# Kernel optimization log

Measured on AMD Instinct MI355X. Metric: run time of the kernel, lower is better.

## Reference

```python
import jax, jax.numpy as jnp
import numpy as np

N_NODES = 100000


def gcn_conv(x, W, b, src, dst, n_nodes):
    """PyG GCNConv: add self-loops, symmetric deg^-1/2 normalization,
    linear transform then gather->scale->scatter-add, plus bias."""
    h = x @ W  # [N, out] - transform first (small GEMM), propagate after
    loop = jnp.arange(n_nodes, dtype=src.dtype)
    s = jnp.concatenate([src, loop])  # sources incl. self-loops
    d = jnp.concatenate([dst, loop])  # targets incl. self-loops
    deg = jax.ops.segment_sum(jnp.ones_like(d, dtype=h.dtype), d,
                              num_segments=n_nodes)  # in-degree on augmented graph
    dinv = jnp.where(deg > 0, jax.lax.rsqrt(deg), 0.0)
    norm = dinv[s] * dinv[d]  # [E+N]
    msg = h[s] * norm[:, None]  # gather + per-edge scale
    out = jax.ops.segment_sum(msg, d, num_segments=n_nodes)  # scatter-add
    return out + b


def setup_inputs() -> dict:
    key = jax.random.key(0)
    ks = jax.random.split(key, 8)
    in_dim, hid = 128, 128
    n_edges = 1600000
    x = jax.random.normal(ks[0], (N_NODES, in_dim), dtype=jnp.float32)
    edge_index = jax.random.randint(ks[1], (2, n_edges), 0, N_NODES, dtype=jnp.int64)
    s1 = 1.0 / np.sqrt(in_dim)
    s2 = 1.0 / np.sqrt(hid)
    W1 = jax.random.uniform(ks[2], (in_dim, hid), jnp.float32, -s1, s1)
    b1 = jnp.zeros((hid,), jnp.float32)
    W2 = jax.random.uniform(ks[3], (hid, 2), jnp.float32, -s2, s2)
    b2 = jnp.zeros((2,), jnp.float32)
    W_skip = jax.random.uniform(ks[4], (in_dim, 2), jnp.float32, -s1, s1)
    b_skip = jnp.zeros((2,), jnp.float32)
    return {"x": x, "edge_index": edge_index, "W1": W1, "b1": b1,
            "W2": W2, "b2": b2, "W_skip": W_skip, "b_skip": b_skip}


def reference(x, edge_index, W1, b1, W2, b2, W_skip, b_skip):
    src, dst = edge_index[0], edge_index[1]
    h = gcn_conv(x, W1, b1, src, dst, N_NODES)
    h = jax.nn.relu(h)
    # dropout is identity in eval mode (training=False)
    out = gcn_conv(h, W2, b2, src, dst, N_NODES)
    out = out + x @ W_skip + b_skip
    return out
```

## Files before the change

kernel.cpp:

```cpp
#include <hip/hip_runtime.h>

#define NN 100000
#define NB 196
#define BSHIFT 9
#define BMASK 511

typedef __attribute__((ext_vector_type(8))) short short8;
typedef __attribute__((ext_vector_type(4))) float f32x4;

__device__ __forceinline__ unsigned short f2bf(float f) {
  union { float f; unsigned int u; } v;
  v.f = f;
  unsigned int r = (v.u + 0x7fffu + ((v.u >> 16) & 1u)) >> 16;
  return (unsigned short)r;
}
__device__ __forceinline__ float bf_lo(unsigned int u) {
  union { unsigned int u; float f; } v;
  v.u = u << 16;
  return v.f;
}
__device__ __forceinline__ float bf_hi(unsigned int u) {
  union { unsigned int u; float f; } v;
  v.u = u & 0xffff0000u;
  return v.f;
}

__global__ __launch_bounds__(256) void k_bucket(const float* __restrict__ W1,
                                                unsigned short* __restrict__ pw,
                                                const int* __restrict__ src,
                                                const int* __restrict__ dst, int E,
                                                int cap, int* __restrict__ bcur,
                                                unsigned int* __restrict__ bkt) {
  if (blockIdx.x < 8) {
    int idx = blockIdx.x * 256 + threadIdx.x;
    int lane = idx & 63, f = idx >> 6;
    int nt = f >> 2, ks = f & 3;
    int n = nt * 16 + (lane & 15);
    int k0 = ks * 32 + (lane >> 4) * 8;
    unsigned short tmp[8];
#pragma unroll
    for (int j = 0; j < 8; ++j) tmp[j] = f2bf(W1[(k0 + j) * 128 + n]);
    *(uint4*)&pw[idx * 8] = *(uint4*)tmp;
    return;
  }
  __shared__ int cnt_l[NB];
  __shared__ int start_l[NB];
  __shared__ int gbase[NB];
  __shared__ unsigned int stage[2048];
  __shared__ int addr[2048];
  const int t = threadIdx.x;
  for (int i = t; i < NB; i += 256) cnt_l[i] = 0;
  __syncthreads();
  const int nblk = gridDim.x - 8;
  const int nbatch = (E + 2047) >> 11;
  for (int bi = blockIdx.x - 8; bi < nbatch; bi += nblk) {
    const int e0 = bi << 11;
    unsigned int ent[8];
    int bb[8], pp[8];
#pragma unroll
    for (int j = 0; j < 8; ++j) {
      int e = e0 + j * 256 + t;
      if (e < E) {
        int d = dst[e], s = src[e];
        bb[j] = d >> BSHIFT;
        ent[j] = ((unsigned int)s << BSHIFT) | (unsigned int)(d & BMASK);
        pp[j] = atomicAdd(&cnt_l[bb[j]], 1);
      } else {
        bb[j] = -1;
      }
    }
    __syncthreads();
    if (t < NB) gbase[t] = atomicAdd(&bcur[t], cnt_l[t]);
    if (t == 0) {
      int run = 0;
      for (int b = 0; b < NB; ++b) { start_l[b] = run; run += cnt_l[b]; }
    }
    __syncthreads();
#pragma unroll
    for (int j = 0; j < 8; ++j) {
      if (bb[j] >= 0) {
        int slot = start_l[bb[j]] + pp[j];
        stage[slot] = ent[j];
        addr[slot] = bb[j] * cap + gbase[bb[j]] + pp[j];
      }
    }
    __syncthreads();
    int totaln = start_l[NB - 1] + cnt_l[NB - 1];
    for (int s = t; s < totaln; s += 256) bkt[addr[s]] = stage[s];
    __syncthreads();
    for (int i = t; i < NB; i += 256) cnt_l[i] = 0;
    __syncthreads();
  }
}

__global__ __launch_bounds__(256) void k_bcount(const int* __restrict__ bcur,
                                                const unsigned int* __restrict__ bkt,
                                                int cap, int* __restrict__ cnt, int n) {
  __shared__ int hist[512];
  const int b = blockIdx.x;
  for (int i = threadIdx.x; i < 512; i += 256) hist[i] = 0;
  __syncthreads();
  const int m = bcur[b];
  const unsigned int* p = &bkt[(size_t)b * cap];
  for (int i = threadIdx.x; i < m; i += 256) atomicAdd(&hist[p[i] & BMASK], 1);
  __syncthreads();
  for (int i = threadIdx.x; i < 512; i += 256) {
    int node = (b << BSHIFT) + i;
    if (node < n) cnt[node] = hist[i];
  }
}

__global__ __launch_bounds__(256) void k_alloc(const int* __restrict__ cnt,
                                               int* __restrict__ ofs,
                                               float* __restrict__ dinv,
                                               int* __restrict__ total, int n) {
  int i = blockIdx.x * 256 + threadIdx.x;
  int c = (i < n) ? cnt[i] : 0;
  int cp = (c + 7) & ~7;
  if (i < n) dinv[i] = rsqrtf((float)c + 1.0f);
  const int lane = threadIdx.x & 63;
  const int wid = threadIdx.x >> 6;
  int incl = cp;
#pragma unroll
  for (int off = 1; off < 64; off <<= 1) {
    int v = __shfl_up(incl, off);
    if (lane >= off) incl += v;
  }
  __shared__ int wsum[4];
  __shared__ int base;
  if (lane == 63) wsum[wid] = incl;
  __syncthreads();
  if (threadIdx.x == 0) {
    int s0 = wsum[0], s1 = wsum[1], s2 = wsum[2], s3 = wsum[3];
    base = atomicAdd(total, s0 + s1 + s2 + s3);
    wsum[0] = 0; wsum[1] = s0; wsum[2] = s0 + s1; wsum[3] = s0 + s1 + s2;
  }
  __syncthreads();
  if (i < n) ofs[i] = base + wsum[wid] + incl - cp;
}

__global__ __launch_bounds__(256) void k_scatter(const int* __restrict__ bcur,
                                                 const unsigned int* __restrict__ bkt,
                                                 int cap, const int* __restrict__ ofs,
                                                 int* __restrict__ bin, int n) {
  __shared__ int cur[512];
  __shared__ int ofs_l[512];
  const int b = blockIdx.x;
  for (int i = threadIdx.x; i < 512; i += 256) {
    cur[i] = 0;
    int node = (b << BSHIFT) + i;
    ofs_l[i] = (node < n) ? ofs[node] : 0;
  }
  __syncthreads();
  const int m = bcur[b];
  const unsigned int* p = &bkt[(size_t)b * cap];
  for (int i = threadIdx.x; i < m; i += 256) {
    unsigned int u = p[i];
    int dl = u & BMASK;
    int pos = atomicAdd(&cur[dl], 1);
    bin[ofs_l[dl] + pos] = (int)(u >> BSHIFT);
  }
  __syncthreads();
  for (int i = threadIdx.x; i < 512; i += 256) {
    int node = (b << BSHIFT) + i;
    if (node < n) {
      int c = cur[i];
      int cp = (c + 7) & ~7;
      int basei = ofs_l[i];
      for (int p2 = c; p2 < cp; ++p2) bin[basei + p2] = n;
    }
  }
}

__global__ __launch_bounds__(256) void k_gemm1(const float* __restrict__ x,
                                               const uint4* __restrict__ pw4,
                                               const float* __restrict__ W_skip,
                                               const float* __restrict__ dinv,
                                               unsigned short* __restrict__ hA16,
                                               float* __restrict__ skipout, int N) {
  __shared__ __align__(16) unsigned short Bs[16384];
  __shared__ float Ws[256];
  const int t = threadIdx.x;
#pragma unroll
  for (int it = 0; it < 8; ++it) {
    int idx = t + it * 256;
    *(uint4*)&Bs[idx * 8] = pw4[idx];
  }
  Ws[t] = W_skip[t];
  __syncthreads();

  const int lane = t & 63, w = t >> 6;
  const int m = lane & 15, q = lane >> 4;
  const int grow = blockIdx.x * 64 + w * 16 + m;
  const bool valid = grow < N;
  const float* xp = &x[(size_t)(valid ? grow : 0) * 128];

  f32x4 acc[8];
#pragma unroll
  for (int nt = 0; nt < 8; ++nt) acc[nt] = (f32x4){0.f, 0.f, 0.f, 0.f};
  float sk0 = 0.f, sk1 = 0.f;

#pragma unroll
  for (int ks = 0; ks < 4; ++ks) {
    short8 a;
    const int kb = ks * 32 + q * 8;
    if (valid) {
      const float* p = xp + kb;
      float4 f0 = *(const float4*)p;
      float4 f1 = *(const float4*)(p + 4);
      a[0] = (short)f2bf(f0.x); a[1] = (short)f2bf(f0.y);
      a[2] = (short)f2bf(f0.z); a[3] = (short)f2bf(f0.w);
      a[4] = (short)f2bf(f1.x); a[5] = (short)f2bf(f1.y);
      a[6] = (short)f2bf(f1.z); a[7] = (short)f2bf(f1.w);
      sk0 += f0.x * Ws[(kb + 0) * 2] + f0.y * Ws[(kb + 1) * 2] +
             f0.z * Ws[(kb + 2) * 2] + f0.w * Ws[(kb + 3) * 2] +
             f1.x * Ws[(kb + 4) * 2] + f1.y * Ws[(kb + 5) * 2] +
             f1.z * Ws[(kb + 6) * 2] + f1.w * Ws[(kb + 7) * 2];
      sk1 += f0.x * Ws[(kb + 0) * 2 + 1] + f0.y * Ws[(kb + 1) * 2 + 1] +
             f0.z * Ws[(kb + 2) * 2 + 1] + f0.w * Ws[(kb + 3) * 2 + 1] +
             f1.x * Ws[(kb + 4) * 2 + 1] + f1.y * Ws[(kb + 5) * 2 + 1] +
             f1.z * Ws[(kb + 6) * 2 + 1] + f1.w * Ws[(kb + 7) * 2 + 1];
    } else {
      a = (short8)0;
    }
#pragma unroll
    for (int nt = 0; nt < 8; ++nt) {
      short8 bfr = *(const short8*)&Bs[((nt * 4 + ks) * 64 + lane) * 8];
      acc[nt] = __builtin_amdgcn_mfma_f32_16x16x32_bf16(a, bfr, acc[nt], 0, 0, 0);
    }
  }

  sk0 += __shfl_xor(sk0, 16); sk0 += __shfl_xor(sk0, 32);
  sk1 += __shfl_xor(sk1, 16); sk1 += __shfl_xor(sk1, 32);
  if (valid && q == 0) *(float2*)&skipout[grow * 2] = make_float2(sk0, sk1);

  const int orow = blockIdx.x * 64 + w * 16 + q * 4;
  float4 dv = *(const float4*)&dinv[orow];
  float dvr[4] = {dv.x, dv.y, dv.z, dv.w};
#pragma unroll
  for (int nt = 0; nt < 8; ++nt) {
    int col = nt * 16 + m;
#pragma unroll
    for (int rg = 0; rg < 4; ++rg) {
      int rr = orow + rg;
      if (rr < N) hA16[(size_t)rr * 128 + col] = f2bf(acc[nt][rg] * dvr[rg]);
    }
  }
}

__global__ __launch_bounds__(256) void k_gather1(const int* __restrict__ ofs,
                                                 const int* __restrict__ cnt,
                                                 const int* __restrict__ bin,
                                                 const float* __restrict__ dinv,
                                                 const uint4* __restrict__ hp,
                                                 const float* __restrict__ b1,
                                                 const float* __restrict__ W2,
                                                 float* __restrict__ t2s, int N) {
  int d = blockIdx.x * 4 + (threadIdx.x >> 6);
  if (d >= N) return;
  const int lane = threadIdx.x & 63;
  const int rg = lane >> 4;
  const int fl = lane & 15;
  const int beg = ofs[d];
  const int np = (cnt[d] + 7) & ~7;

  const float dd = dinv[d];
  uint4 vs = hp[(size_t)d * 16 + fl];
  float4 b1a = *(const float4*)&b1[fl * 8];
  float4 b1b = *(const float4*)&b1[fl * 8 + 4];
  float4 wa = *(const float4*)&W2[fl * 16];
  float4 wb = *(const float4*)&W2[fl * 16 + 4];
  float4 wc = *(const float4*)&W2[fl * 16 + 8];
  float4 wd = *(const float4*)&W2[fl * 16 + 12];

  float acc[8] = {};
  for (int e0 = 0; e0 < np; e0 += 8) {
    int s0 = bin[beg + e0 + rg];
    int s1 = bin[beg + e0 + 4 + rg];
    uint4 v0 = hp[(size_t)s0 * 16 + fl];
    uint4 v1 = hp[(size_t)s1 * 16 + fl];
    acc[0] += bf_lo(v0.x); acc[1] += bf_hi(v0.x);
    acc[2] += bf_lo(v0.y); acc[3] += bf_hi(v0.y);
    acc[4] += bf_lo(v0.z); acc[5] += bf_hi(v0.z);
    acc[6] += bf_lo(v0.w); acc[7] += bf_hi(v0.w);
    acc[0] += bf_lo(v1.x); acc[1] += bf_hi(v1.x);
    acc[2] += bf_lo(v1.y); acc[3] += bf_hi(v1.y);
    acc[4] += bf_lo(v1.z); acc[5] += bf_hi(v1.z);
    acc[6] += bf_lo(v1.w); acc[7] += bf_hi(v1.w);
  }
#pragma unroll
  for (int j = 0; j < 8; ++j) {
    acc[j] += __shfl_xor(acc[j], 16);
    acc[j] += __shfl_xor(acc[j], 32);
  }
  acc[0] += bf_lo(vs.x); acc[1] += bf_hi(vs.x);
  acc[2] += bf_lo(vs.y); acc[3] += bf_hi(vs.y);
  acc[4] += bf_lo(vs.z); acc[5] += bf_hi(vs.z);
  acc[6] += bf_lo(vs.w); acc[7] += bf_hi(vs.w);

  float vj[8];
  vj[0] = fmaxf(acc[0] * dd + b1a.x, 0.f);
  vj[1] = fmaxf(acc[1] * dd + b1a.y, 0.f);
  vj[2] = fmaxf(acc[2] * dd + b1a.z, 0.f);
  vj[3] = fmaxf(acc[3] * dd + b1a.w, 0.f);
  vj[4] = fmaxf(acc[4] * dd + b1b.x, 0.f);
  vj[5] = fmaxf(acc[5] * dd + b1b.y, 0.f);
  vj[6] = fmaxf(acc[6] * dd + b1b.z, 0.f);
  vj[7] = fmaxf(acc[7] * dd + b1b.w, 0.f);
  float p0 = vj[0] * wa.x + vj[1] * wa.z + vj[2] * wb.x + vj[3] * wb.z +
             vj[4] * wc.x + vj[5] * wc.z + vj[6] * wd.x + vj[7] * wd.z;
  float p1 = vj[0] * wa.y + vj[1] * wa.w + vj[2] * wb.y + vj[3] * wb.w +
             vj[4] * wc.y + vj[5] * wc.w + vj[6] * wd.y + vj[7] * wd.w;
#pragma unroll
  for (int off = 1; off < 16; off <<= 1) {
    p0 += __shfl_xor(p0, off);
    p1 += __shfl_xor(p1, off);
  }
  if (lane == 0) *(float2*)&t2s[d * 2] = make_float2(p0 * dd, p1 * dd);
}

__global__ __launch_bounds__(256) void k_final(const float* __restrict__ b_skip,
                                               const float* __restrict__ b2,
                                               const float* __restrict__ t2s,
                                               const float* __restrict__ skipout,
                                               const float* __restrict__ dinv,
                                               const int* __restrict__ ofs,
                                               const int* __restrict__ cnt,
                                               const int* __restrict__ bin,
                                               float* __restrict__ out, int N) {
  int i = blockIdx.x * 4 + (threadIdx.x >> 6);
  if (i >= N) return;
  const int lane = threadIdx.x & 63;
  const int beg = ofs[i], end = beg + cnt[i];
  float g0 = 0.f, g1 = 0.f;
  for (int e = beg + lane; e < end; e += 64) {
    int s = bin[e];
    float2 t = *(const float2*)&t2s[s * 2];
    g0 += t.x; g1 += t.y;
  }
#pragma unroll
  for (int off = 32; off > 0; off >>= 1) {
    g0 += __shfl_down(g0, off);
    g1 += __shfl_down(g1, off);
  }
  if (lane == 0) {
    float di = dinv[i];
    float2 ts = *(const float2*)&t2s[i * 2];
    float2 sk = *(const float2*)&skipout[i * 2];
    float o0 = di * (g0 + ts.x) + b2[0] + sk.x + b_skip[0];
    float o1 = di * (g1 + ts.y) + b2[1] + sk.y + b_skip[1];
    *(float2*)&out[i * 2] = make_float2(o0, o1);
  }
}

extern "C" void kernel_launch(void* const* d_in, const int* in_sizes, int n_in,
                              void* d_out, int out_size, void* d_ws, size_t ws_size,
                              hipStream_t stream) {
  const float* x      = (const float*)d_in[0];
  const int*   edges  = (const int*)d_in[1];
  const float* W1     = (const float*)d_in[2];
  const float* b1     = (const float*)d_in[3];
  const float* W2     = (const float*)d_in[4];
  const float* b2     = (const float*)d_in[5];
  const float* W_skip = (const float*)d_in[6];
  const float* b_skip = (const float*)d_in[7];
  float* out = (float*)d_out;

  const int N = NN;
  const int E = in_sizes[1] / 2;
  const int* src = edges;
  const int* dst = edges + E;
  const size_t BINCAP = (size_t)E + 8 * (size_t)N;
  const int CAP = (((E + NB - 1) / NB) + 1280 + 255) & ~255;

  unsigned short* hA16 = (unsigned short*)d_ws;
  int*   bcur    = (int*)(hA16 + (size_t)(NN + 1) * 128);
  int*   total   = bcur + NB;
  int*   ofs     = total + 4;
  float* dinv    = (float*)(ofs + N + 4);
  int*   cnt     = (int*)(dinv + N);
  unsigned int* bkt = (unsigned int*)(cnt + N);
  int*   bin     = (int*)(bkt + (size_t)NB * CAP);
  float* t2s     = (float*)(bin + BINCAP);
  float* skipout = t2s + 2 * (size_t)N;
  unsigned short* pw = (unsigned short*)(skipout + 2 * (size_t)N);

  hipMemsetAsync(hA16 + (size_t)N * 128, 0, 256 + (NB + 4) * sizeof(int), stream);

  k_bucket<<<8 + 392, 256, 0, stream>>>(W1, pw, src, dst, E, CAP, bcur, bkt);
  k_bcount<<<NB, 256, 0, stream>>>(bcur, bkt, CAP, cnt, N);
  k_alloc<<<(N + 255) / 256, 256, 0, stream>>>(cnt, ofs, dinv, total, N);
  k_scatter<<<NB, 256, 0, stream>>>(bcur, bkt, CAP, ofs, bin, N);
  k_gemm1<<<(N + 63) / 64, 256, 0, stream>>>(x, (const uint4*)pw, W_skip, dinv, hA16,
                                             skipout, N);
  k_gather1<<<(N + 3) / 4, 256, 0, stream>>>(ofs, cnt, bin, dinv, (const uint4*)hA16,
                                             b1, W2, t2s, N);
  k_final<<<(N + 3) / 4, 256, 0, stream>>>(b_skip, b2, t2s, skipout, dinv, ofs, cnt,
                                           bin, out, N);
}
```

Baseline: 267.6 us.

## Fuse CSR count/alloc/scatter kernels, parallel-scan bucket offsets, packed-add gather

Merges the bucket-count, offset-allocation and scatter kernels into one per-bucket kernel that builds the histogram, scans padded counts, writes ofs/cnt/dinv and fills bins. This removes two launches and a global round-trip of the counts. The serial per-batch prefix loop in k_bucket becomes a wave shuffle scan, and the bucket grid is doubled. Padding grows to 16 so the layer-1 gather handles four neighbours per iteration with v_pk_add_f32 packed accumulation. The cost is more padding slots in the bin array and more gather loads on padded zero rows.

```diff
diff --git a/kernel.cpp b/kernel.cpp
--- a/kernel.cpp
+++ b/kernel.cpp
@@ -7,6 +7,7 @@
 
 typedef __attribute__((ext_vector_type(8))) short short8;
 typedef __attribute__((ext_vector_type(4))) float f32x4;
+typedef __attribute__((ext_vector_type(2))) float f32x2;
 
 __device__ __forceinline__ unsigned short f2bf(float f) {
   union { float f; unsigned int u; } v;
@@ -23,6 +24,18 @@
   union { unsigned int u; float f; } v;
   v.u = u & 0xffff0000u;
   return v.f;
+}
+__device__ __forceinline__ f32x2 mk2(unsigned int u) {
+  union { unsigned int u; float f; } lo, hi;
+  lo.u = u << 16;
+  hi.u = u & 0xffff0000u;
+  f32x2 r;
+  r.x = lo.f;
+  r.y = hi.f;
+  return r;
+}
+__device__ __forceinline__ void pkadd(f32x2& a, f32x2 b) {
+  asm("v_pk_add_f32 %0, %0, %1" : "+v"(a) : "v"(b));
 }
 
 __global__ __launch_bounds__(256) void k_bucket(const float* __restrict__ W1,
@@ -46,9 +59,11 @@
   __shared__ int cnt_l[NB];
   __shared__ int start_l[NB];
   __shared__ int gbase[NB];
+  __shared__ int wsum2[4];
   __shared__ unsigned int stage[2048];
   __shared__ int addr[2048];
   const int t = threadIdx.x;
+  const int lane = t & 63, wid = t >> 6;
   for (int i = t; i < NB; i += 256) cnt_l[i] = 0;
   __syncthreads();
   const int nblk = gridDim.x - 8;
@@ -70,11 +85,21 @@
       }
     }
     __syncthreads();
-    if (t < NB) gbase[t] = atomicAdd(&bcur[t], cnt_l[t]);
-    if (t == 0) {
-      int run = 0;
-      for (int b = 0; b < NB; ++b) { start_l[b] = run; run += cnt_l[b]; }
-    }
+    int v = (t < NB) ? cnt_l[t] : 0;
+    if (t < NB) gbase[t] = atomicAdd(&bcur[t], v);
+    int incl = v;
+#pragma unroll
+    for (int off = 1; off < 64; off <<= 1) {
+      int u = __shfl_up(incl, off);
+      if (lane >= off) incl += u;
+    }
+    if (lane == 63) wsum2[wid] = incl;
+    __syncthreads();
+    int wpre = 0;
+#pragma unroll
+    for (int j = 0; j < 4; ++j) wpre += (j < wid) ? wsum2[j] : 0;
+    int tot = wsum2[0] + wsum2[1] + wsum2[2] + wsum2[3];
+    if (t < NB) start_l[t] = wpre + incl - v;
     __syncthreads();
 #pragma unroll
     for (int j = 0; j < 8; ++j) {
@@ -85,90 +110,75 @@
       }
     }
     __syncthreads();
-    int totaln = start_l[NB - 1] + cnt_l[NB - 1];
-    for (int s = t; s < totaln; s += 256) bkt[addr[s]] = stage[s];
+    for (int s2 = t; s2 < tot; s2 += 256) bkt[addr[s2]] = stage[s2];
     __syncthreads();
     for (int i = t; i < NB; i += 256) cnt_l[i] = 0;
     __syncthreads();
   }
 }
 
-__global__ __launch_bounds__(256) void k_bcount(const int* __restrict__ bcur,
-                                                const unsigned int* __restrict__ bkt,
-                                                int cap, int* __restrict__ cnt, int n) {
+__global__ __launch_bounds__(256) void k_scatter(const int* __restrict__ bcur,
+                                                 const unsigned int* __restrict__ bkt,
+                                                 int cap, int* __restrict__ total,
+                                                 int* __restrict__ ofs,
+                                                 int* __restrict__ cnt,
+                                                 float* __restrict__ dinv,
+                                                 int* __restrict__ bin, int n) {
   __shared__ int hist[512];
+  __shared__ int sofs[512];
+  __shared__ int wsum[4];
+  __shared__ int base;
   const int b = blockIdx.x;
-  for (int i = threadIdx.x; i < 512; i += 256) hist[i] = 0;
+  const int t = threadIdx.x;
+  const int lane = t & 63, wid = t >> 6;
+  hist[2 * t] = 0;
+  hist[2 * t + 1] = 0;
   __syncthreads();
   const int m = bcur[b];
   const unsigned int* p = &bkt[(size_t)b * cap];
-  for (int i = threadIdx.x; i < m; i += 256) atomicAdd(&hist[p[i] & BMASK], 1);
-  __syncthreads();
-  for (int i = threadIdx.x; i < 512; i += 256) {
-    int node = (b << BSHIFT) + i;
-    if (node < n) cnt[node] = hist[i];
-  }
-}
-
-__global__ __launch_bounds__(256) void k_alloc(const int* __restrict__ cnt,
-                                               int* __restrict__ ofs,
-                                               float* __restrict__ dinv,
-                                               int* __restrict__ total, int n) {
-  int i = blockIdx.x * 256 + threadIdx.x;
-  int c = (i < n) ? cnt[i] : 0;
-  int cp = (c + 7) & ~7;
-  if (i < n) dinv[i] = rsqrtf((float)c + 1.0f);
-  const int lane = threadIdx.x & 63;
-  const int wid = threadIdx.x >> 6;
-  int incl = cp;
+  for (int i = t; i < m; i += 256) atomicAdd(&hist[p[i] & BMASK], 1);
+  __syncthreads();
+  int c0 = hist[2 * t], c1 = hist[2 * t + 1];
+  int cp0 = (c0 + 15) & ~15, cp1 = (c1 + 15) & ~15;
+  int v = cp0 + cp1;
+  int incl = v;
 #pragma unroll
   for (int off = 1; off < 64; off <<= 1) {
-    int v = __shfl_up(incl, off);
-    if (lane >= off) incl += v;
-  }
-  __shared__ int wsum[4];
-  __shared__ int base;
+    int u = __shfl_up(incl, off);
+    if (lane >= off) incl += u;
+  }
   if (lane == 63) wsum[wid] = incl;
   __syncthreads();
-  if (threadIdx.x == 0) {
+  if (t == 0) {
     int s0 = wsum[0], s1 = wsum[1], s2 = wsum[2], s3 = wsum[3];
     base = atomicAdd(total, s0 + s1 + s2 + s3);
     wsum[0] = 0; wsum[1] = s0; wsum[2] = s0 + s1; wsum[3] = s0 + s1 + s2;
   }
   __syncthreads();
-  if (i < n) ofs[i] = base + wsum[wid] + incl - cp;
-}
-
-__global__ __launch_bounds__(256) void k_scatter(const int* __restrict__ bcur,
-                                                 const unsigned int* __restrict__ bkt,
-                                                 int cap, const int* __restrict__ ofs,
-                                                 int* __restrict__ bin, int n) {
-  __shared__ int cur[512];
-  __shared__ int ofs_l[512];
-  const int b = blockIdx.x;
-  for (int i = threadIdx.x; i < 512; i += 256) {
-    cur[i] = 0;
-    int node = (b << BSHIFT) + i;
-    ofs_l[i] = (node < n) ? ofs[node] : 0;
-  }
-  __syncthreads();
-  const int m = bcur[b];
-  const unsigned int* p = &bkt[(size_t)b * cap];
-  for (int i = threadIdx.x; i < m; i += 256) {
+  int exc = base + wsum[wid] + incl - v;
+  sofs[2 * t] = exc;
+  sofs[2 * t + 1] = exc + cp0;
+  int node = (b << BSHIFT) + 2 * t;
+  if (node < n) {
+    ofs[node] = exc;
+    cnt[node] = c0;
+    dinv[node] = rsqrtf((float)c0 + 1.0f);
+  }
+  if (node + 1 < n) {
+    ofs[node + 1] = exc + cp0;
+    cnt[node + 1] = c1;
+    dinv[node + 1] = rsqrtf((float)c1 + 1.0f);
+  }
+  hist[2 * t] = 0;
+  hist[2 * t + 1] = 0;
+  __syncthreads();
+  for (int p2 = c0; p2 < cp0; ++p2) bin[exc + p2] = n;
+  for (int p2 = c1; p2 < cp1; ++p2) bin[exc + cp0 + p2] = n;
+  for (int i = t; i < m; i += 256) {
     unsigned int u = p[i];
     int dl = u & BMASK;
-    int pos = atomicAdd(&cur[dl], 1);
-    bin[ofs_l[dl] + pos] = (int)(u >> BSHIFT);
-  }
-  __syncthreads();
-  for (int i = threadIdx.x; i < 512; i += 256) {
-    int node = (b << BSHIFT) + i;
-    if (node < n) {
-      int c = cur[i];
-      int cp = (c + 7) & ~7;
-      int basei = ofs_l[i];
-      for (int p2 = c; p2 < cp; ++p2) bin[basei + p2] = n;
-    }
+    int pos = atomicAdd(&hist[dl], 1);
+    bin[sofs[dl] + pos] = (int)(u >> BSHIFT);
   }
 }
 
@@ -262,7 +272,7 @@
   const int rg = lane >> 4;
   const int fl = lane & 15;
   const int beg = ofs[d];
-  const int np = (cnt[d] + 7) & ~7;
+  const int np = (cnt[d] + 15) & ~15;
 
   const float dd = dinv[d];
   uint4 vs = hp[(size_t)d * 16 + fl];
@@ -273,21 +283,31 @@
   float4 wc = *(const float4*)&W2[fl * 16 + 8];
   float4 wd = *(const float4*)&W2[fl * 16 + 12];
 
-  float acc[8] = {};
-  for (int e0 = 0; e0 < np; e0 += 8) {
-    int s0 = bin[beg + e0 + rg];
-    int s1 = bin[beg + e0 + 4 + rg];
+  f32x2 a2[4];
+#pragma unroll
+  for (int j = 0; j < 4; ++j) a2[j] = (f32x2){0.f, 0.f};
+
+  for (int e0 = 0; e0 < np; e0 += 16) {
+    int eb = beg + e0 + rg;
+    int s0 = bin[eb], s1 = bin[eb + 4], s2 = bin[eb + 8], s3 = bin[eb + 12];
     uint4 v0 = hp[(size_t)s0 * 16 + fl];
     uint4 v1 = hp[(size_t)s1 * 16 + fl];
-    acc[0] += bf_lo(v0.x); acc[1] += bf_hi(v0.x);
-    acc[2] += bf_lo(v0.y); acc[3] += bf_hi(v0.y);
-    acc[4] += bf_lo(v0.z); acc[5] += bf_hi(v0.z);
-    acc[6] += bf_lo(v0.w); acc[7] += bf_hi(v0.w);
-    acc[0] += bf_lo(v1.x); acc[1] += bf_hi(v1.x);
-    acc[2] += bf_lo(v1.y); acc[3] += bf_hi(v1.y);
-    acc[4] += bf_lo(v1.z); acc[5] += bf_hi(v1.z);
-    acc[6] += bf_lo(v1.w); acc[7] += bf_hi(v1.w);
-  }
+    uint4 v2 = hp[(size_t)s2 * 16 + fl];
+    uint4 v3 = hp[(size_t)s3 * 16 + fl];
+    pkadd(a2[0], mk2(v0.x)); pkadd(a2[1], mk2(v0.y));
+    pkadd(a2[2], mk2(v0.z)); pkadd(a2[3], mk2(v0.w));
+    pkadd(a2[0], mk2(v1.x)); pkadd(a2[1], mk2(v1.y));
+    pkadd(a2[2], mk2(v1.z)); pkadd(a2[3], mk2(v1.w));
+    pkadd(a2[0], mk2(v2.x)); pkadd(a2[1], mk2(v2.y));
+    pkadd(a2[2], mk2(v2.z)); pkadd(a2[3], mk2(v2.w));
+    pkadd(a2[0], mk2(v3.x)); pkadd(a2[1], mk2(v3.y));
+    pkadd(a2[2], mk2(v3.z)); pkadd(a2[3], mk2(v3.w));
+  }
+  float acc[8];
+  acc[0] = a2[0].x; acc[1] = a2[0].y;
+  acc[2] = a2[1].x; acc[3] = a2[1].y;
+  acc[4] = a2[2].x; acc[5] = a2[2].y;
+  acc[6] = a2[3].x; acc[7] = a2[3].y;
 #pragma unroll
   for (int j = 0; j < 8; ++j) {
     acc[j] += __shfl_xor(acc[j], 16);
@@ -370,7 +390,7 @@
   const int E = in_sizes[1] / 2;
   const int* src = edges;
   const int* dst = edges + E;
-  const size_t BINCAP = (size_t)E + 8 * (size_t)N;
+  const size_t BINCAP = (size_t)E + 16 * (size_t)N;
   const int CAP = (((E + NB - 1) / NB) + 1280 + 255) & ~255;
 
   unsigned short* hA16 = (unsigned short*)d_ws;
@@ -387,10 +407,8 @@
 
   hipMemsetAsync(hA16 + (size_t)N * 128, 0, 256 + (NB + 4) * sizeof(int), stream);
 
-  k_bucket<<<8 + 392, 256, 0, stream>>>(W1, pw, src, dst, E, CAP, bcur, bkt);
-  k_bcount<<<NB, 256, 0, stream>>>(bcur, bkt, CAP, cnt, N);
-  k_alloc<<<(N + 255) / 256, 256, 0, stream>>>(cnt, ofs, dinv, total, N);
-  k_scatter<<<NB, 256, 0, stream>>>(bcur, bkt, CAP, ofs, bin, N);
+  k_bucket<<<8 + 784, 256, 0, stream>>>(W1, pw, src, dst, E, CAP, bcur, bkt);
+  k_scatter<<<NB, 256, 0, stream>>>(bcur, bkt, CAP, total, ofs, cnt, dinv, bin, N);
   k_gemm1<<<(N + 63) / 64, 256, 0, stream>>>(x, (const uint4*)pw, W_skip, dinv, hA16,
                                              skipout, N);
   k_gather1<<<(N + 3) / 4, 256, 0, stream>>>(ofs, cnt, bin, dinv, (const uint4*)hA16,
```

Result: no change. 265.0 us (-1.0%).

## Fuse bucket count, offset allocation and scatter; parallelize bucket prefix scan

Applied to the files above, without the earlier changes.

Merges the per-bucket histogram, offset allocation (with dinv) and scatter into one 512-thread kernel per bucket, reading each bucket's entries from its local histogram. The serial single-thread prefix over 196 buckets in the bucketing kernel becomes a wave-shuffle scan. Bucketing also moves to 512-thread blocks with 4096-edge batches and one block per batch. This removes two kernel launches and a global round trip for counts and offsets. In exchange, node offsets are allocated in bucket-block order rather than a global node order.

```diff
diff --git a/kernel.cpp b/kernel.cpp
--- a/kernel.cpp
+++ b/kernel.cpp
@@ -25,14 +25,14 @@
   return v.f;
 }
 
-__global__ __launch_bounds__(256) void k_bucket(const float* __restrict__ W1,
+__global__ __launch_bounds__(512) void k_bucket(const float* __restrict__ W1,
                                                 unsigned short* __restrict__ pw,
                                                 const int* __restrict__ src,
                                                 const int* __restrict__ dst, int E,
                                                 int cap, int* __restrict__ bcur,
                                                 unsigned int* __restrict__ bkt) {
-  if (blockIdx.x < 8) {
-    int idx = blockIdx.x * 256 + threadIdx.x;
+  if (blockIdx.x < 4) {
+    int idx = blockIdx.x * 512 + threadIdx.x;
     int lane = idx & 63, f = idx >> 6;
     int nt = f >> 2, ks = f & 3;
     int n = nt * 16 + (lane & 15);
@@ -46,20 +46,22 @@
   __shared__ int cnt_l[NB];
   __shared__ int start_l[NB];
   __shared__ int gbase[NB];
-  __shared__ unsigned int stage[2048];
-  __shared__ int addr[2048];
+  __shared__ int wsum2[8];
+  __shared__ unsigned int stage[4096];
+  __shared__ int addr[4096];
   const int t = threadIdx.x;
-  for (int i = t; i < NB; i += 256) cnt_l[i] = 0;
-  __syncthreads();
-  const int nblk = gridDim.x - 8;
-  const int nbatch = (E + 2047) >> 11;
-  for (int bi = blockIdx.x - 8; bi < nbatch; bi += nblk) {
-    const int e0 = bi << 11;
+  const int lane = t & 63, wid = t >> 6;
+  for (int i = t; i < NB; i += 512) cnt_l[i] = 0;
+  __syncthreads();
+  const int nblk = gridDim.x - 4;
+  const int nbatch = (E + 4095) >> 12;
+  for (int bi = blockIdx.x - 4; bi < nbatch; bi += nblk) {
+    const int e0 = bi << 12;
     unsigned int ent[8];
     int bb[8], pp[8];
 #pragma unroll
     for (int j = 0; j < 8; ++j) {
-      int e = e0 + j * 256 + t;
+      int e = e0 + j * 512 + t;
       if (e < E) {
         int d = dst[e], s = src[e];
         bb[j] = d >> BSHIFT;
@@ -70,11 +72,22 @@
       }
     }
     __syncthreads();
-    if (t < NB) gbase[t] = atomicAdd(&bcur[t], cnt_l[t]);
-    if (t == 0) {
-      int run = 0;
-      for (int b = 0; b < NB; ++b) { start_l[b] = run; run += cnt_l[b]; }
-    }
+    int v = (t < NB) ? cnt_l[t] : 0;
+    if (t < NB) gbase[t] = atomicAdd(&bcur[t], v);
+    int incl = v;
+#pragma unroll
+    for (int off = 1; off < 64; off <<= 1) {
+      int u = __shfl_up(incl, off);
+      if (lane >= off) incl += u;
+    }
+    if (lane == 63) wsum2[wid] = incl;
+    __syncthreads();
+    int wpre = 0;
+#pragma unroll
+    for (int j = 0; j < 8; ++j) wpre += (j < wid) ? wsum2[j] : 0;
+    int tot = wsum2[0] + wsum2[1] + wsum2[2] + wsum2[3] +
+              wsum2[4] + wsum2[5] + wsum2[6] + wsum2[7];
+    if (t < NB) start_l[t] = wpre + incl - v;
     __syncthreads();
 #pragma unroll
     for (int j = 0; j < 8; ++j) {
@@ -85,90 +98,66 @@
       }
     }
     __syncthreads();
-    int totaln = start_l[NB - 1] + cnt_l[NB - 1];
-    for (int s = t; s < totaln; s += 256) bkt[addr[s]] = stage[s];
-    __syncthreads();
-    for (int i = t; i < NB; i += 256) cnt_l[i] = 0;
-    __syncthreads();
-  }
-}
-
-__global__ __launch_bounds__(256) void k_bcount(const int* __restrict__ bcur,
-                                                const unsigned int* __restrict__ bkt,
-                                                int cap, int* __restrict__ cnt, int n) {
+    for (int s2 = t; s2 < tot; s2 += 512) bkt[addr[s2]] = stage[s2];
+    __syncthreads();
+    for (int i = t; i < NB; i += 512) cnt_l[i] = 0;
+    __syncthreads();
+  }
+}
+
+__global__ __launch_bounds__(512) void k_scatter(const int* __restrict__ bcur,
+                                                 const unsigned int* __restrict__ bkt,
+                                                 int cap, int* __restrict__ total,
+                                                 int* __restrict__ ofs,
+                                                 int* __restrict__ cnt,
+                                                 float* __restrict__ dinv,
+                                                 int* __restrict__ bin, int n) {
   __shared__ int hist[512];
+  __shared__ int sofs[512];
+  __shared__ int wsum[8];
+  __shared__ int base;
   const int b = blockIdx.x;
-  for (int i = threadIdx.x; i < 512; i += 256) hist[i] = 0;
+  const int t = threadIdx.x;
+  const int lane = t & 63, wid = t >> 6;
+  hist[t] = 0;
   __syncthreads();
   const int m = bcur[b];
   const unsigned int* p = &bkt[(size_t)b * cap];
-  for (int i = threadIdx.x; i < m; i += 256) atomicAdd(&hist[p[i] & BMASK], 1);
-  __syncthreads();
-  for (int i = threadIdx.x; i < 512; i += 256) {
-    int node = (b << BSHIFT) + i;
-    if (node < n) cnt[node] = hist[i];
-  }
-}
-
-__global__ __launch_bounds__(256) void k_alloc(const int* __restrict__ cnt,
-                                               int* __restrict__ ofs,
-                                               float* __restrict__ dinv,
-                                               int* __restrict__ total, int n) {
-  int i = blockIdx.x * 256 + threadIdx.x;
-  int c = (i < n) ? cnt[i] : 0;
+  for (int i = t; i < m; i += 512) atomicAdd(&hist[p[i] & BMASK], 1);
+  __syncthreads();
+  int c = hist[t];
   int cp = (c + 7) & ~7;
-  if (i < n) dinv[i] = rsqrtf((float)c + 1.0f);
-  const int lane = threadIdx.x & 63;
-  const int wid = threadIdx.x >> 6;
   int incl = cp;
 #pragma unroll
   for (int off = 1; off < 64; off <<= 1) {
-    int v = __shfl_up(incl, off);
-    if (lane >= off) incl += v;
-  }
-  __shared__ int wsum[4];
-  __shared__ int base;
+    int u = __shfl_up(incl, off);
+    if (lane >= off) incl += u;
+  }
   if (lane == 63) wsum[wid] = incl;
   __syncthreads();
-  if (threadIdx.x == 0) {
-    int s0 = wsum[0], s1 = wsum[1], s2 = wsum[2], s3 = wsum[3];
-    base = atomicAdd(total, s0 + s1 + s2 + s3);
-    wsum[0] = 0; wsum[1] = s0; wsum[2] = s0 + s1; wsum[3] = s0 + s1 + s2;
-  }
-  __syncthreads();
-  if (i < n) ofs[i] = base + wsum[wid] + incl - cp;
-}
-
-__global__ __launch_bounds__(256) void k_scatter(const int* __restrict__ bcur,
-                                                 const unsigned int* __restrict__ bkt,
-                                                 int cap, const int* __restrict__ ofs,
-                                                 int* __restrict__ bin, int n) {
-  __shared__ int cur[512];
-  __shared__ int ofs_l[512];
-  const int b = blockIdx.x;
-  for (int i = threadIdx.x; i < 512; i += 256) {
-    cur[i] = 0;
-    int node = (b << BSHIFT) + i;
-    ofs_l[i] = (node < n) ? ofs[node] : 0;
-  }
-  __syncthreads();
-  const int m = bcur[b];
-  const unsigned int* p = &bkt[(size_t)b * cap];
-  for (int i = threadIdx.x; i < m; i += 256) {
+  if (t == 0) {
+    int run = 0;
+#pragma unroll
+    for (int j = 0; j < 8; ++j) { int s = wsum[j]; wsum[j] = run; run += s; }
+    base = atomicAdd(total, run);
+  }
+  __syncthreads();
+  int exc = base + wsum[wid] + incl - cp;
+  sofs[t] = exc;
+  int node = (b << BSHIFT) + t;
+  if (node < n) {
+    ofs[node] = exc;
+    cnt[node] = c;
+    dinv[node] = rsqrtf((float)c + 1.0f);
+  }
+  hist[t] = 0;
+  __syncthreads();
+  for (int p2 = c; p2 < cp; ++p2) bin[exc + p2] = n;
+  for (int i = t; i < m; i += 512) {
     unsigned int u = p[i];
     int dl = u & BMASK;
-    int pos = atomicAdd(&cur[dl], 1);
-    bin[ofs_l[dl] + pos] = (int)(u >> BSHIFT);
-  }
-  __syncthreads();
-  for (int i = threadIdx.x; i < 512; i += 256) {
-    int node = (b << BSHIFT) + i;
-    if (node < n) {
-      int c = cur[i];
-      int cp = (c + 7) & ~7;
-      int basei = ofs_l[i];
-      for (int p2 = c; p2 < cp; ++p2) bin[basei + p2] = n;
-    }
+    int pos = atomicAdd(&hist[dl], 1);
+    bin[sofs[dl] + pos] = (int)(u >> BSHIFT);
   }
 }
 
@@ -387,10 +376,9 @@
 
   hipMemsetAsync(hA16 + (size_t)N * 128, 0, 256 + (NB + 4) * sizeof(int), stream);
 
-  k_bucket<<<8 + 392, 256, 0, stream>>>(W1, pw, src, dst, E, CAP, bcur, bkt);
-  k_bcount<<<NB, 256, 0, stream>>>(bcur, bkt, CAP, cnt, N);
-  k_alloc<<<(N + 255) / 256, 256, 0, stream>>>(cnt, ofs, dinv, total, N);
-  k_scatter<<<NB, 256, 0, stream>>>(bcur, bkt, CAP, ofs, bin, N);
+  const int nbatch = (E + 4095) / 4096;
+  k_bucket<<<4 + nbatch, 512, 0, stream>>>(W1, pw, src, dst, E, CAP, bcur, bkt);
+  k_scatter<<<NB, 512, 0, stream>>>(bcur, bkt, CAP, total, ofs, cnt, dinv, bin, N);
   k_gemm1<<<(N + 63) / 64, 256, 0, stream>>>(x, (const uint4*)pw, W_skip, dinv, hA16,
                                              skipout, N);
   k_gather1<<<(N + 3) / 4, 256, 0, stream>>>(ofs, cnt, bin, dinv, (const uint4*)hA16,
```

Measured after the change: 245.4 us. -8.3%, faster.
